# Kernel tuning notes

Measured on AMD Instinct MI355X. Metric: run time of the kernel, lower is better.

Reference implementation:

```python
import jax, jax.numpy as jnp
import numpy as np

XBOUND = (-51.2, 51.2, 0.8)
YBOUND = (-51.2, 51.2, 0.8)
ZBOUND = (-10.0, 10.0, 20.0)
DBOUND = (1.0, 60.0, 1.0)
IMG_H, IMG_W = 256, 704
DOWNSAMPLE = 16
CAM_C = 64
OUT_C = 64
D = int((DBOUND[1] - DBOUND[0]) / DBOUND[2])      # 59
NX = int((XBOUND[1] - XBOUND[0]) / XBOUND[2])     # 128
NY = int((YBOUND[1] - YBOUND[0]) / YBOUND[2])     # 128
NZ = int((ZBOUND[1] - ZBOUND[0]) / ZBOUND[2])     # 1
FH, FW = IMG_H // DOWNSAMPLE, IMG_W // DOWNSAMPLE # 16, 44
DX = jnp.array([XBOUND[2], YBOUND[2], ZBOUND[2]], dtype=jnp.float32)
BX = jnp.array([XBOUND[0] + XBOUND[2] / 2.0, YBOUND[0] + YBOUND[2] / 2.0, ZBOUND[0] + ZBOUND[2] / 2.0], dtype=jnp.float32)


def make_frustum():
    ds = jnp.arange(DBOUND[0], DBOUND[1], DBOUND[2], dtype=jnp.float32)   # [D]
    xs = jnp.linspace(0.0, IMG_W - 1.0, FW, dtype=jnp.float32)            # [FW]
    ys = jnp.linspace(0.0, IMG_H - 1.0, FH, dtype=jnp.float32)            # [FH]
    d = jnp.broadcast_to(ds[:, None, None], (D, FH, FW))
    x = jnp.broadcast_to(xs[None, None, :], (D, FH, FW))
    y = jnp.broadcast_to(ys[None, :, None], (D, FH, FW))
    return jnp.stack([x, y, d], axis=-1)                                  # [D,FH,FW,3]


def get_geometry(rots, trans, intrins, post_rots, post_trans):
    # rots/intrins/post_rots: [B,N,3,3]; trans/post_trans: [B,N,3]
    frustum = make_frustum()                                              # [D,FH,FW,3]
    pts = frustum[None, None] - post_trans[:, :, None, None, None]        # [B,N,D,FH,FW,3]
    pts = jnp.einsum('bnij,bndhwj->bndhwi', jnp.linalg.inv(post_rots), pts)
    pts = jnp.concatenate([pts[..., :2] * pts[..., 2:3], pts[..., 2:3]], axis=-1)
    comb = jnp.matmul(rots, jnp.linalg.inv(intrins))
    pts = jnp.einsum('bnij,bndhwj->bndhwi', comb, pts)
    return pts + trans[:, :, None, None, None]


def forward(x, rots, trans, intrins, post_rots, post_trans, w_depth, b_depth):
    B, N, C_in, H, W = x.shape
    # 1x1 conv == channel matmul
    y = jnp.einsum('bnchw,oc->bnohw', x, w_depth) + b_depth[None, None, :, None, None]
    depth = jax.nn.softmax(y[:, :, :D], axis=2)              # [B,N,D,H,W]
    context = y[:, :, D:]                                    # [B,N,OUT_C,H,W]
    outer = depth[:, :, :, None] * context[:, :, None, :]    # [B,N,D,OUT_C,H,W]
    outer = jnp.transpose(outer, (0, 1, 2, 4, 5, 3))         # [B,N,D,H,W,OUT_C]

    geom = jax.lax.stop_gradient(get_geometry(rots, trans, intrins, post_rots, post_trans))
    # torch .long() truncates toward zero -> jnp.trunc
    g = jnp.trunc((geom.reshape(-1, 3) - (BX - DX / 2.0)) / DX).astype(jnp.int32)  # [P,3]
    kept = ((g[:, 0] >= 0) & (g[:, 0] < NX) &
            (g[:, 1] >= 0) & (g[:, 1] < NY) &
            (g[:, 2] >= 0) & (g[:, 2] < NZ))
    batch_ix = jnp.repeat(jnp.arange(B, dtype=jnp.int32), N * D * H * W)
    ranks = batch_ix * (NX * NY * NZ) + g[:, 0] + g[:, 1] * NX + g[:, 2] * NX * NY
    # segment-sum over voxel ranks == sort+cumsum trick + scatter in the original
    feats = jnp.where(kept[:, None], outer.reshape(-1, OUT_C), 0.0)
    ranks = jnp.where(kept, ranks, 0)
    bev = jax.ops.segment_sum(feats, ranks, num_segments=B * NZ * NY * NX)
    bev = bev.reshape(B, NZ, NY, NX, OUT_C).transpose(0, 4, 1, 2, 3).sum(axis=2)
    return bev  # [B, OUT_C, NY, NX]


def setup_inputs() -> dict:
    key = jax.random.key(0)
    B, N = 4, 6
    ks = jax.random.split(key, 8)
    cam2ego = jnp.array([[0.0, 0.0, 1.0], [-1.0, 0.0, 0.0], [0.0, -1.0, 0.0]], dtype=jnp.float32)
    rots = jnp.broadcast_to(cam2ego, (B, N, 3, 3)) + 0.02 * jax.random.normal(ks[0], (B, N, 3, 3), dtype=jnp.float32)
    trans = 1.0 * jax.random.normal(ks[1], (B, N, 3), dtype=jnp.float32)
    K = jnp.array([[700.0, 0.0, IMG_W / 2.0], [0.0, 700.0, IMG_H / 2.0], [0.0, 0.0, 1.0]], dtype=jnp.float32)
    intrins = jnp.broadcast_to(K, (B, N, 3, 3)) + 0.1 * jax.random.normal(ks[2], (B, N, 3, 3), dtype=jnp.float32)
    post_rots = jnp.broadcast_to(jnp.eye(3, dtype=jnp.float32), (B, N, 3, 3)) + 0.01 * jax.random.normal(ks[3], (B, N, 3, 3), dtype=jnp.float32)
    post_trans = 0.1 * jax.random.normal(ks[4], (B, N, 3), dtype=jnp.float32)
    x = jax.random.normal(ks[5], (B, N, CAM_C, FH, FW), dtype=jnp.float32)
    w_depth = 0.05 * jax.random.normal(ks[6], (D + OUT_C, CAM_C), dtype=jnp.float32)
    b_depth = jnp.zeros((D + OUT_C,), dtype=jnp.float32)
    return {"x": x, "rots": rots, "trans": trans, "intrins": intrins,
            "post_rots": post_rots, "post_trans": post_trans,
            "w_depth": w_depth, "b_depth": b_depth}


def reference(x, rots, trans, intrins, post_rots, post_trans, w_depth, b_depth):
    return forward(x, rots, trans, intrins, post_rots, post_trans, w_depth, b_depth)
```

## Files before the change

kernel.cpp:

```cpp
#include <hip/hip_runtime.h>
#include <math.h>

#define Bc 4
#define Nc 6
#define Dc 59
#define FHc 16
#define FWc 44
#define Cc 64
#define OCc 123
#define NXc 128
#define NYc 128
#define NVOX (Bc*NXc*NYc)
#define NBLK (Bc*Nc*FWc)

#define WS_ACC 0
#define WS_CAM ((size_t)16777216)

template<bool FMA>
__device__ __forceinline__ float mulsub(float a, float b, float c) {
    if (FMA) return __fmaf_rn(-a, b, c);
    return __fadd_rn(c, __fmul_rn(-a, b));
}

template<bool FMA>
__device__ __forceinline__ void lu_inv3x3T(const float* __restrict__ m, float* __restrict__ o) {
    float A[3][3] = {{m[0],m[3],m[6]},{m[1],m[4],m[7]},{m[2],m[5],m[8]}};
    int piv0, piv1;
    {
        float a0=fabsf(A[0][0]), a1=fabsf(A[1][0]), a2=fabsf(A[2][0]);
        int p = 0; float mx = a0;
        if (a1 > mx) { mx = a1; p = 1; }
        if (a2 > mx) { mx = a2; p = 2; }
        piv0 = p;
        if (p != 0) { for (int k=0;k<3;++k){ float t=A[0][k]; A[0][k]=A[p][k]; A[p][k]=t; } }
        const float d = __fdiv_rn(1.0f, A[0][0]);
        A[1][0] = __fmul_rn(A[1][0], d);
        A[2][0] = __fmul_rn(A[2][0], d);
        #pragma unroll
        for (int i=1;i<3;++i)
            #pragma unroll
            for (int j=1;j<3;++j)
                A[i][j] = mulsub<FMA>(A[i][0], A[0][j], A[i][j]);
    }
    {
        float a1=fabsf(A[1][1]), a2=fabsf(A[2][1]);
        int p = (a2 > a1) ? 2 : 1;
        piv1 = p;
        if (p != 1) { for (int k=0;k<3;++k){ float t=A[1][k]; A[1][k]=A[p][k]; A[p][k]=t; } }
        const float d = __fdiv_rn(1.0f, A[1][1]);
        A[2][1] = __fmul_rn(A[2][1], d);
        A[2][2] = mulsub<FMA>(A[2][1], A[1][2], A[2][2]);
    }
    float B[3][3] = {{1.f,0.f,0.f},{0.f,1.f,0.f},{0.f,0.f,1.f}};
    if (piv0 != 0) { for (int k=0;k<3;++k){ float t=B[0][k]; B[0][k]=B[piv0][k]; B[piv0][k]=t; } }
    if (piv1 != 1) { for (int k=0;k<3;++k){ float t=B[1][k]; B[1][k]=B[piv1][k]; B[piv1][k]=t; } }
    #pragma unroll
    for (int j=0;j<3;++j) {
        B[1][j] = mulsub<FMA>(A[1][0], B[0][j], B[1][j]);
        B[2][j] = mulsub<FMA>(A[2][0], B[0][j], B[2][j]);
        B[2][j] = mulsub<FMA>(A[2][1], B[1][j], B[2][j]);
        B[2][j] = __fdiv_rn(B[2][j], A[2][2]);
        B[0][j] = mulsub<FMA>(A[0][2], B[2][j], B[0][j]);
        B[1][j] = mulsub<FMA>(A[1][2], B[2][j], B[1][j]);
        B[1][j] = __fdiv_rn(B[1][j], A[1][1]);
        B[0][j] = mulsub<FMA>(A[0][1], B[1][j], B[0][j]);
        B[0][j] = __fdiv_rn(B[0][j], A[0][0]);
    }
    o[0]=B[0][0]; o[1]=B[1][0]; o[2]=B[2][0];
    o[3]=B[0][1]; o[4]=B[1][1]; o[5]=B[2][1];
    o[6]=B[0][2]; o[7]=B[1][2]; o[8]=B[2][2];
}

template<bool FMA>
__device__ __forceinline__ float dot3(float a0,float a1,float a2,float b0,float b1,float b2){
    if (FMA) return __fmaf_rn(a2,b2, __fmaf_rn(a1,b1, __fmul_rn(a0,b0)));
    return __fadd_rn(__fadd_rn(__fmul_rn(a0,b0), __fmul_rn(a1,b1)), __fmul_rn(a2,b2));
}

__global__ __launch_bounds__(64) void cam_precompute(
    const float* __restrict__ rots, const float* __restrict__ intrins,
    const float* __restrict__ post_rots, float* __restrict__ camMat)
{
    const int t = threadIdx.x;
    if (t >= 48) return;
    const int cam = t >> 1;
    const int var = t & 1;
    const float* pr = post_rots + cam*9;
    const float* ro = rots      + cam*9;
    const float* it = intrins   + cam*9;
    float PRi[9], INi[9], CM[9];
    if (var == 0) { lu_inv3x3T<true >(pr, PRi); lu_inv3x3T<true >(it, INi); }
    else          { lu_inv3x3T<false>(pr, PRi); lu_inv3x3T<false>(it, INi); }
    #pragma unroll
    for (int r2 = 0; r2 < 3; ++r2)
        #pragma unroll
        for (int c2 = 0; c2 < 3; ++c2)
            CM[r2*3+c2] = dot3<true>(ro[r2*3+0], ro[r2*3+1], ro[r2*3+2],
                                     INi[0*3+c2], INi[1*3+c2], INi[2*3+c2]);
    float* dst = camMat + (size_t)(cam*2 + var)*18;
    #pragma unroll
    for (int k = 0; k < 9; ++k) { dst[k] = PRi[k]; dst[9+k] = CM[k]; }
}

template<bool FMA>
__device__ __forceinline__ int geom_light(
    const float* __restrict__ PRi, const float* __restrict__ CM,
    float pt0, float pt1, float pt2, float tr0, float tr1, float tr2,
    float u, float v, float dval, int b)
{
    const float p0 = __fsub_rn(u,    pt0);
    const float p1 = __fsub_rn(v,    pt1);
    const float p2 = __fsub_rn(dval, pt2);
    const float q0 = dot3<FMA>(PRi[0],PRi[1],PRi[2], p0,p1,p2);
    const float q1 = dot3<FMA>(PRi[3],PRi[4],PRi[5], p0,p1,p2);
    const float q2 = dot3<FMA>(PRi[6],PRi[7],PRi[8], p0,p1,p2);
    const float r0 = __fmul_rn(q0, q2);
    const float r1 = __fmul_rn(q1, q2);
    const float s0 = __fadd_rn(dot3<FMA>(CM[0],CM[1],CM[2], r0,r1,q2), tr0);
    const float s1 = __fadd_rn(dot3<FMA>(CM[3],CM[4],CM[5], r0,r1,q2), tr1);
    const float s2 = __fadd_rn(dot3<FMA>(CM[6],CM[7],CM[8], r0,r1,q2), tr2);
    const float CX  = -51.200000762939453f;
    const float DXf =  0.80000001192092896f;
    const float gx = __fdiv_rn(__fsub_rn(s0, CX), DXf);
    const float gy = __fdiv_rn(__fsub_rn(s1, CX), DXf);
    const float gz = __fdiv_rn(__fsub_rn(s2, -10.0f), 20.0f);
    const bool kept = (gx > -1.0f) && (gx < 128.0f) &&
                      (gy > -1.0f) && (gy < 128.0f) &&
                      (gz > -1.0f) && (gz < 1.0f);
    return kept ? (b*(NXc*NYc) + ((int)gy)*NXc + (int)gx) : -1;
}

__global__ __launch_bounds__(256) void lss_main(
    const float* __restrict__ x, const float* __restrict__ trans,
    const float* __restrict__ post_trans,
    const float* __restrict__ wd, const float* __restrict__ bd,
    const float* __restrict__ camMat, float* __restrict__ acc)
{
    const int blk = blockIdx.x;
    const int wi  = blk % FWc;
    const int cam = blk / FWc;
    const int b   = cam / Nc;
    const int t = threadIdx.x;
    const int wave = t >> 6, lane = t & 63;

    __shared__ float xs[16][64];
    __shared__ float yv[16][124];
    __shared__ int   voxA[16][Dc];
    __shared__ int   voxB[16][Dc];

    {
        const float* xb = x + (size_t)cam*64*FHc*FWc + wi;
        for (int idx = t; idx < 1024; idx += 256) {
            const int c = idx & 63, hi = idx >> 6;
            xs[hi][c] = xb[(size_t)c*(FHc*FWc) + hi*FWc];
        }
    }
    __syncthreads();

    for (int idx = t; idx < 16*OCc; idx += 256) {
        const int hi = idx / OCc, o = idx - hi*OCc;
        const float* wr = wd + o*Cc;
        float a = 0.0f;
        #pragma unroll
        for (int c2 = 0; c2 < Cc; ++c2)
            a = __fmaf_rn(wr[c2], xs[hi][c2], a);
        yv[hi][o] = __fadd_rn(a, bd[o]);
    }
    __syncthreads();

    for (int k = 0; k < 4; ++k) {
        const int hi = (wave << 2) | k;
        float v = (lane < Dc) ? yv[hi][lane] : -INFINITY;
        float m = v;
        #pragma unroll
        for (int off = 32; off; off >>= 1) m = fmaxf(m, __shfl_xor(m, off));
        float e = (lane < Dc) ? expf(__fsub_rn(v, m)) : 0.0f;
        float s = e;
        #pragma unroll
        for (int off = 32; off; off >>= 1) s = __fadd_rn(s, __shfl_xor(s, off));
        if (lane < Dc) yv[hi][lane] = __fdiv_rn(e, s);
    }

    {
        const float pt0 = post_trans[cam*3+0], pt1 = post_trans[cam*3+1], pt2 = post_trans[cam*3+2];
        const float tr0 = trans[cam*3+0],      tr1 = trans[cam*3+1],      tr2 = trans[cam*3+2];
        const float* M0 = camMat + (size_t)(cam*2 + 0)*18;
        const float* M1 = camMat + (size_t)(cam*2 + 1)*18;
        const float u = (float)(wi * (703.0 / 43.0));
        for (int idx = t; idx < 16*Dc; idx += 256) {
            const int hi = idx / Dc, d = idx - hi*Dc;
            const float v    = (float)(hi * 17.0);
            const float dval = (float)(1 + d);
            voxA[hi][d] = geom_light<true >(M0, M0+9, pt0,pt1,pt2, tr0,tr1,tr2, u, v, dval, b);
            voxB[hi][d] = geom_light<false>(M1, M1+9, pt0,pt1,pt2, tr0,tr1,tr2, u, v, dval, b);
        }
    }
    __syncthreads();

    for (int d = wave; d < Dc; d += 4) {
        int runVox = -1;
        float accv = 0.0f;
        #pragma unroll
        for (int hi = 0; hi < 16; ++hi) {
            const int vA = voxA[hi][d];
            const int vB = voxB[hi][d];
            const float dw = yv[hi][d];
            const float cx = yv[hi][59 + lane];
            if (vA == vB) {
                if (vA >= 0) {
                    if (vA != runVox) {
                        if (runVox >= 0) atomicAdd(&acc[((size_t)runVox << 6) + lane], accv);
                        runVox = vA; accv = 0.0f;
                    }
                    accv = __fadd_rn(accv, __fmul_rn(dw, cx));
                }
            } else {
                const float hw = __fmul_rn(dw, 0.5f);
                if (vA >= 0) {
                    if (vA != runVox) {
                        if (runVox >= 0) atomicAdd(&acc[((size_t)runVox << 6) + lane], accv);
                        runVox = vA; accv = 0.0f;
                    }
                    accv = __fadd_rn(accv, __fmul_rn(hw, cx));
                }
                if (vB >= 0) atomicAdd(&acc[((size_t)vB << 6) + lane], __fmul_rn(hw, cx));
            }
        }
        if (runVox >= 0) atomicAdd(&acc[((size_t)runVox << 6) + lane], accv);
    }
}

__global__ __launch_bounds__(256) void lss_transpose(
    const float* __restrict__ acc, float* __restrict__ out)
{
    __shared__ float tile[64][65];
    const int blk = blockIdx.x;
    const int b = blk >> 8;
    const int pixbase = (blk & 255) * 64;
    const float* src = acc + ((size_t)b*16384 + pixbase)*64;
    const int t = threadIdx.x;
    #pragma unroll
    for (int i = 0; i < 16; ++i) {
        const int e = i*256 + t;
        tile[e & 63][e >> 6] = src[e];
    }
    __syncthreads();
    float* dst = out + (size_t)b*64*16384 + pixbase;
    #pragma unroll
    for (int i = 0; i < 16; ++i) {
        const int e = i*256 + t;
        const int c = e >> 6, p = e & 63;
        dst[(size_t)c*16384 + p] = tile[c][p];
    }
}

extern "C" void kernel_launch(void* const* d_in, const int* in_sizes, int n_in,
                              void* d_out, int out_size, void* d_ws, size_t ws_size,
                              hipStream_t stream) {
    const float* x          = (const float*)d_in[0];
    const float* rots       = (const float*)d_in[1];
    const float* trans      = (const float*)d_in[2];
    const float* intrins    = (const float*)d_in[3];
    const float* post_rots  = (const float*)d_in[4];
    const float* post_trans = (const float*)d_in[5];
    const float* wd         = (const float*)d_in[6];
    const float* bd         = (const float*)d_in[7];
    float* out = (float*)d_out;
    char* ws = (char*)d_ws;

    float* acc    = (float*)(ws + WS_ACC);
    float* camMat = (float*)(ws + WS_CAM);

    hipMemsetAsync(acc, 0, (size_t)NVOX*64*sizeof(float), stream);
    cam_precompute<<<dim3(1), dim3(64), 0, stream>>>(rots, intrins, post_rots, camMat);
    lss_main<<<dim3(NBLK), dim3(256), 0, stream>>>(
        x, trans, post_trans, wd, bd, camMat, acc);
    lss_transpose<<<dim3(Bc*256), dim3(256), 0, stream>>>(acc, out);
}
```

Baseline: 227.9 us.

## Register-block depth conv with pre-transposed weights and pack per-depth geometry in LDS

```diff
diff --git a/kernel.cpp b/kernel.cpp
--- a/kernel.cpp
+++ b/kernel.cpp
@@ -15,6 +15,7 @@
 
 #define WS_ACC 0
 #define WS_CAM ((size_t)16777216)
+#define WS_WDT ((size_t)16781312)
 
 template<bool FMA>
 __device__ __forceinline__ float mulsub(float a, float b, float c) {
@@ -77,29 +78,35 @@
     return __fadd_rn(__fadd_rn(__fmul_rn(a0,b0), __fmul_rn(a1,b1)), __fmul_rn(a2,b2));
 }
 
-__global__ __launch_bounds__(64) void cam_precompute(
-    const float* __restrict__ rots, const float* __restrict__ intrins,
-    const float* __restrict__ post_rots, float* __restrict__ camMat)
+__global__ __launch_bounds__(256) void prep(
+    const float* __restrict__ wd, const float* __restrict__ rots,
+    const float* __restrict__ intrins, const float* __restrict__ post_rots,
+    float* __restrict__ wdT, float* __restrict__ camMat)
 {
-    const int t = threadIdx.x;
-    if (t >= 48) return;
-    const int cam = t >> 1;
-    const int var = t & 1;
-    const float* pr = post_rots + cam*9;
-    const float* ro = rots      + cam*9;
-    const float* it = intrins   + cam*9;
-    float PRi[9], INi[9], CM[9];
-    if (var == 0) { lu_inv3x3T<true >(pr, PRi); lu_inv3x3T<true >(it, INi); }
-    else          { lu_inv3x3T<false>(pr, PRi); lu_inv3x3T<false>(it, INi); }
-    #pragma unroll
-    for (int r2 = 0; r2 < 3; ++r2)
-        #pragma unroll
-        for (int c2 = 0; c2 < 3; ++c2)
-            CM[r2*3+c2] = dot3<true>(ro[r2*3+0], ro[r2*3+1], ro[r2*3+2],
-                                     INi[0*3+c2], INi[1*3+c2], INi[2*3+c2]);
-    float* dst = camMat + (size_t)(cam*2 + var)*18;
-    #pragma unroll
-    for (int k = 0; k < 9; ++k) { dst[k] = PRi[k]; dst[9+k] = CM[k]; }
+    const int idx = blockIdx.x*256 + threadIdx.x;
+    if (idx < OCc*Cc) {
+        const int o = idx >> 6, c = idx & 63;
+        wdT[(c << 7) + o] = wd[idx];
+    }
+    if (blockIdx.x == 0 && threadIdx.x < 48) {
+        const int cam = threadIdx.x >> 1;
+        const int var = threadIdx.x & 1;
+        const float* pr = post_rots + cam*9;
+        const float* ro = rots      + cam*9;
+        const float* it = intrins   + cam*9;
+        float PRi[9], INi[9], CM[9];
+        if (var == 0) { lu_inv3x3T<true >(pr, PRi); lu_inv3x3T<true >(it, INi); }
+        else          { lu_inv3x3T<false>(pr, PRi); lu_inv3x3T<false>(it, INi); }
+        #pragma unroll
+        for (int r2 = 0; r2 < 3; ++r2)
+            #pragma unroll
+            for (int c2 = 0; c2 < 3; ++c2)
+                CM[r2*3+c2] = dot3<true>(ro[r2*3+0], ro[r2*3+1], ro[r2*3+2],
+                                         INi[0*3+c2], INi[1*3+c2], INi[2*3+c2]);
+        float* dst = camMat + (size_t)(cam*2 + var)*18;
+        #pragma unroll
+        for (int k = 0; k < 9; ++k) { dst[k] = PRi[k]; dst[9+k] = CM[k]; }
+    }
 }
 
 template<bool FMA>
@@ -132,9 +139,9 @@
 
 __global__ __launch_bounds__(256) void lss_main(
     const float* __restrict__ x, const float* __restrict__ trans,
-    const float* __restrict__ post_trans,
-    const float* __restrict__ wd, const float* __restrict__ bd,
-    const float* __restrict__ camMat, float* __restrict__ acc)
+    const float* __restrict__ post_trans, const float* __restrict__ bd,
+    const float* __restrict__ wdT, const float* __restrict__ camMat,
+    float* __restrict__ acc)
 {
     const int blk = blockIdx.x;
     const int wi  = blk % FWc;
@@ -143,31 +150,46 @@
     const int t = threadIdx.x;
     const int wave = t >> 6, lane = t & 63;
 
-    __shared__ float xs[16][64];
-    __shared__ float yv[16][124];
-    __shared__ int   voxA[16][Dc];
-    __shared__ int   voxB[16][Dc];
-
-    {
-        const float* xb = x + (size_t)cam*64*FHc*FWc + wi;
+    __shared__ float  xsT[64][16];
+    __shared__ float  yv[16][60];
+    __shared__ float  ctxT[64][18];
+    __shared__ float4 geo[Dc][16];
+
+    {
+        const float* xb = x + (size_t)cam*64*(FHc*FWc) + wi;
         for (int idx = t; idx < 1024; idx += 256) {
-            const int c = idx & 63, hi = idx >> 6;
-            xs[hi][c] = xb[(size_t)c*(FHc*FWc) + hi*FWc];
+            const int c = idx >> 4, hi = idx & 15;
+            xsT[c][hi] = xb[(size_t)c*(FHc*FWc) + hi*FWc];
         }
     }
     __syncthreads();
 
-    for (int idx = t; idx < 16*OCc; idx += 256) {
-        const int hi = idx / OCc, o = idx - hi*OCc;
-        const float* wr = wd + o*Cc;
-        float a = 0.0f;
-        #pragma unroll
-        for (int c2 = 0; c2 < Cc; ++c2)
-            a = __fmaf_rn(wr[c2], xs[hi][c2], a);
-        yv[hi][o] = __fadd_rn(a, bd[o]);
-    }
-    __syncthreads();
-
+    {
+        const int hi0 = wave << 2;
+        float a0[4] = {0.f,0.f,0.f,0.f}, a1[4] = {0.f,0.f,0.f,0.f};
+        for (int c = 0; c < 64; ++c) {
+            const float w0 = wdT[(c << 7) + lane];
+            const float w1 = wdT[(c << 7) + 64 + lane];
+            const float4 xv = *(const float4*)&xsT[c][hi0];
+            a0[0] = __fmaf_rn(w0, xv.x, a0[0]); a1[0] = __fmaf_rn(w1, xv.x, a1[0]);
+            a0[1] = __fmaf_rn(w0, xv.y, a0[1]); a1[1] = __fmaf_rn(w1, xv.y, a1[1]);
+            a0[2] = __fmaf_rn(w0, xv.z, a0[2]); a1[2] = __fmaf_rn(w1, xv.z, a1[2]);
+            a0[3] = __fmaf_rn(w0, xv.w, a0[3]); a1[3] = __fmaf_rn(w1, xv.w, a1[3]);
+        }
+        const float b0 = bd[lane];
+        const float b1 = (lane < 59) ? bd[64 + lane] : 0.0f;
+        #pragma unroll
+        for (int k = 0; k < 4; ++k) {
+            const int hi = hi0 + k;
+            const float y0 = __fadd_rn(a0[k], b0);
+            if (lane < 59) {
+                yv[hi][lane] = y0;
+                ctxT[lane + 5][hi] = __fadd_rn(a1[k], b1);
+            } else {
+                ctxT[lane - 59][hi] = y0;
+            }
+        }
+    }
     for (int k = 0; k < 4; ++k) {
         const int hi = (wave << 2) | k;
         float v = (lane < Dc) ? yv[hi][lane] : -INFINITY;
@@ -180,6 +202,7 @@
         for (int off = 32; off; off >>= 1) s = __fadd_rn(s, __shfl_xor(s, off));
         if (lane < Dc) yv[hi][lane] = __fdiv_rn(e, s);
     }
+    __syncthreads();
 
     {
         const float pt0 = post_trans[cam*3+0], pt1 = post_trans[cam*3+1], pt2 = post_trans[cam*3+2];
@@ -188,45 +211,55 @@
         const float* M1 = camMat + (size_t)(cam*2 + 1)*18;
         const float u = (float)(wi * (703.0 / 43.0));
         for (int idx = t; idx < 16*Dc; idx += 256) {
-            const int hi = idx / Dc, d = idx - hi*Dc;
+            const int d = idx >> 4, hi = idx & 15;
             const float v    = (float)(hi * 17.0);
             const float dval = (float)(1 + d);
-            voxA[hi][d] = geom_light<true >(M0, M0+9, pt0,pt1,pt2, tr0,tr1,tr2, u, v, dval, b);
-            voxB[hi][d] = geom_light<false>(M1, M1+9, pt0,pt1,pt2, tr0,tr1,tr2, u, v, dval, b);
+            const int vA = geom_light<true >(M0, M0+9, pt0,pt1,pt2, tr0,tr1,tr2, u, v, dval, b);
+            const int vB = geom_light<false>(M1, M1+9, pt0,pt1,pt2, tr0,tr1,tr2, u, v, dval, b);
+            geo[d][hi] = make_float4(yv[hi][d], __int_as_float(vA), __int_as_float(vB), 0.0f);
         }
     }
     __syncthreads();
 
-    for (int d = wave; d < Dc; d += 4) {
-        int runVox = -1;
-        float accv = 0.0f;
-        #pragma unroll
-        for (int hi = 0; hi < 16; ++hi) {
-            const int vA = voxA[hi][d];
-            const int vB = voxB[hi][d];
-            const float dw = yv[hi][d];
-            const float cx = yv[hi][59 + lane];
-            if (vA == vB) {
-                if (vA >= 0) {
-                    if (vA != runVox) {
-                        if (runVox >= 0) atomicAdd(&acc[((size_t)runVox << 6) + lane], accv);
-                        runVox = vA; accv = 0.0f;
+    {
+        float cx[16];
+        #pragma unroll
+        for (int h = 0; h < 16; h += 2) {
+            const float2 c2 = *(const float2*)&ctxT[lane][h];
+            cx[h] = c2.x; cx[h+1] = c2.y;
+        }
+        for (int d = wave; d < Dc; d += 4) {
+            int runVox = -1;
+            float accv = 0.0f;
+            #pragma unroll
+            for (int hi = 0; hi < 16; ++hi) {
+                const float4 g = geo[d][hi];
+                const float dw = g.x;
+                const int vA = __float_as_int(g.y);
+                const int vB = __float_as_int(g.z);
+                const float cxv = cx[hi];
+                if (vA == vB) {
+                    if (vA >= 0) {
+                        if (vA != runVox) {
+                            if (runVox >= 0) atomicAdd(&acc[((size_t)runVox << 6) + lane], accv);
+                            runVox = vA; accv = 0.0f;
+                        }
+                        accv = __fadd_rn(accv, __fmul_rn(dw, cxv));
                     }
-                    accv = __fadd_rn(accv, __fmul_rn(dw, cx));
+                } else {
+                    const float hw = __fmul_rn(dw, 0.5f);
+                    if (vA >= 0) {
+                        if (vA != runVox) {
+                            if (runVox >= 0) atomicAdd(&acc[((size_t)runVox << 6) + lane], accv);
+                            runVox = vA; accv = 0.0f;
+                        }
+                        accv = __fadd_rn(accv, __fmul_rn(hw, cxv));
+                    }
+                    if (vB >= 0) atomicAdd(&acc[((size_t)vB << 6) + lane], __fmul_rn(hw, cxv));
                 }
-            } else {
-                const float hw = __fmul_rn(dw, 0.5f);
-                if (vA >= 0) {
-                    if (vA != runVox) {
-                        if (runVox >= 0) atomicAdd(&acc[((size_t)runVox << 6) + lane], accv);
-                        runVox = vA; accv = 0.0f;
-                    }
-                    accv = __fadd_rn(accv, __fmul_rn(hw, cx));
-                }
-                if (vB >= 0) atomicAdd(&acc[((size_t)vB << 6) + lane], __fmul_rn(hw, cx));
             }
-        }
-        if (runVox >= 0) atomicAdd(&acc[((size_t)runVox << 6) + lane], accv);
+            if (runVox >= 0) atomicAdd(&acc[((size_t)runVox << 6) + lane], accv);
+        }
     }
 }
 
@@ -270,10 +303,11 @@
 
     float* acc    = (float*)(ws + WS_ACC);
     float* camMat = (float*)(ws + WS_CAM);
+    float* wdT    = (float*)(ws + WS_WDT);
 
     hipMemsetAsync(acc, 0, (size_t)NVOX*64*sizeof(float), stream);
-    cam_precompute<<<dim3(1), dim3(64), 0, stream>>>(rots, intrins, post_rots, camMat);
+    prep<<<dim3(31), dim3(256), 0, stream>>>(wd, rots, intrins, post_rots, wdT, camMat);
     lss_main<<<dim3(NBLK), dim3(256), 0, stream>>>(
-        x, trans, post_trans, wd, bd, camMat, acc);
+        x, trans, post_trans, bd, wdT, camMat, acc);
     lss_transpose<<<dim3(Bc*256), dim3(256), 0, stream>>>(acc, out);
 }
```

New measurement: 261.7 us. 14.8% more time.
